# Performance work log

Hardware: AMD Instinct MI355X
Metric: run time of the kernel (lower is better)

The kernel has to match this reference:

```python
import jax, jax.numpy as jnp
import numpy as np
import math

N, S, T, E, H = 2, 2048, 2048, 1024, 16
HD = E // H  # head_dim = 64


def setup_inputs() -> dict:
    key = jax.random.key(0)
    ks = jax.random.split(key, 11)
    scale = 1.0 / math.sqrt(E)
    inp = {
        "query": jax.random.normal(ks[0], (N, S, E), jnp.float32),
        "key": jax.random.normal(ks[1], (N, T, E), jnp.float32),
        "value": jax.random.normal(ks[2], (N, T, E), jnp.float32),
        "Wq": jax.random.normal(ks[3], (E, E), jnp.float32) * scale,
        "bq": jnp.zeros((E,), jnp.float32),
        "Wk": jax.random.normal(ks[4], (E, E), jnp.float32) * scale,
        "bk": jnp.zeros((E,), jnp.float32),
        "Wv": jax.random.normal(ks[5], (E, E), jnp.float32) * scale,
        "bv": jnp.zeros((E,), jnp.float32),
        "Wo": jax.random.normal(ks[6], (E, E), jnp.float32) * scale,
        "bo": jnp.zeros((E,), jnp.float32),
    }
    return inp


def reference(query, key, value, Wq, bq, Wk, bk, Wv, bv, Wo, bo):
    # QKV projections, then split heads: [N, S, E] -> [N, H, S, HD]
    q = (query @ Wq + bq).reshape(N, S, H, HD).transpose(0, 2, 1, 3)
    k = (key @ Wk + bk).reshape(N, T, H, HD).transpose(0, 2, 1, 3)
    v = (value @ Wv + bv).reshape(N, T, H, HD).transpose(0, 2, 1, 3)
    # scaled dot-product attention scores [N, H, S, T]
    scores = jnp.einsum('nhse,nhte->nhst', q, k) / math.sqrt(HD)
    attn = jax.nn.softmax(scores, axis=-1)
    # dropout is identity in eval mode
    out = jnp.einsum('nhst,nhte->nhse', attn, v)  # [N, H, S, HD]
    out = out.transpose(0, 2, 1, 3).reshape(N, S, E)
    return out @ Wo + bo
```

## Files before the change

### kernel.cpp

```cpp
#include <hip/hip_runtime.h>
#include <hip/hip_bf16.h>

typedef __bf16 bf16x8 __attribute__((ext_vector_type(8)));
typedef __bf16 bf16x4 __attribute__((ext_vector_type(4)));
typedef float  f32x4  __attribute__((ext_vector_type(4)));
typedef float  f32x16 __attribute__((ext_vector_type(16)));

#define MFMA16(a, b, c) __builtin_amdgcn_mfma_f32_16x16x32_bf16((a), (b), (c), 0, 0, 0)
#define MFMA32(a, b, c) __builtin_amdgcn_mfma_f32_32x32x16_bf16((a), (b), (c), 0, 0, 0)

constexpr int SEQ = 2048, EMB = 1024, NHEAD = 16, HD = 64;
constexpr float SSCALE = 0.18033688f;

__device__ __forceinline__ void glds16(const void* g, void* l) {
    __builtin_amdgcn_global_load_lds(
        (const __attribute__((address_space(1))) void*)g,
        (__attribute__((address_space(3))) void*)l, 16, 0, 0);
}

__global__ __launch_bounds__(256)
void prep(const float* __restrict__ W0, const float* __restrict__ W1,
          const float* __restrict__ W2, const float* __restrict__ W3,
          __bf16* __restrict__ T0, __bf16* __restrict__ T1,
          __bf16* __restrict__ T2, __bf16* __restrict__ T3,
          const float* __restrict__ X0, const float* __restrict__ X1,
          const float* __restrict__ X2, __bf16* __restrict__ Y0,
          __bf16* __restrict__ Y1, __bf16* __restrict__ Y2)
{
    __shared__ float tile[32][33];
    const int z = blockIdx.z;
    if (z < 4) {
        const float* W = (z==0) ? W0 : (z==1) ? W1 : (z==2) ? W2 : W3;
        __bf16*      T = (z==0) ? T0 : (z==1) ? T1 : (z==2) ? T2 : T3;
        const float s = (z == 0) ? SSCALE : 1.0f;
        const int kb = blockIdx.x * 32, nb = blockIdx.y * 32;
        const int c = threadIdx.x & 31, r0 = threadIdx.x >> 5;
#pragma unroll
        for (int i = 0; i < 4; ++i)
            tile[r0 + 8*i][c] = W[(size_t)(kb + r0 + 8*i)*1024 + nb + c];
        __syncthreads();
#pragma unroll
        for (int i = 0; i < 4; ++i)
            T[(size_t)(nb + r0 + 8*i)*1024 + kb + c] = (__bf16)(tile[c][r0 + 8*i] * s);
    } else {
        const float* X = (z==4) ? X0 : (z==5) ? X1 : X2;
        __bf16*      Y = (z==4) ? Y0 : (z==5) ? Y1 : Y2;
        const size_t base =
            ((size_t)(blockIdx.y * 32 + blockIdx.x) * 256 + threadIdx.x) * 16;
#pragma unroll
        for (int j = 0; j < 2; ++j) {
            const float4* s4 = (const float4*)(X + base + j*8);
            float4 f0 = s4[0], f1 = s4[1];
            bf16x8 v;
            v[0]=(__bf16)f0.x; v[1]=(__bf16)f0.y; v[2]=(__bf16)f0.z; v[3]=(__bf16)f0.w;
            v[4]=(__bf16)f1.x; v[5]=(__bf16)f1.y; v[6]=(__bf16)f1.z; v[7]=(__bf16)f1.w;
            *(bf16x8*)(Y + base + j*8) = v;
        }
    }
}

struct GArg { const __bf16* A; const __bf16* Bt; const float* bias; void* C;
              int mode; int kbase; int kcount; float bscale; };
struct GArgs3 { GArg a[3]; };

__global__ __launch_bounds__(256)
void gemmk(GArgs3 args)
{
    const GArg g = args.a[blockIdx.z];
    __shared__ __attribute__((aligned(16))) __bf16 As[128*64];
    __shared__ __attribute__((aligned(16))) __bf16 Bs[128*64];
    const int tid = threadIdx.x, lane = tid & 63, wave = tid >> 6;
    const int wm = wave >> 1, wn = wave & 1;
    const int quad = lane >> 4, l16 = lane & 15;
    const int bm = blockIdx.x, bn = blockIdx.y;

    f32x4 acc[4][4] = {};

    for (int kt = 0; kt < g.kcount; ++kt) {
        const int k0 = g.kbase + kt*64;
        __syncthreads();
#pragma unroll
        for (int j = 0; j < 4; ++j) {
            const int ci = j*256 + tid;
            const int row = ci >> 3, cg = ((ci & 7) ^ (row & 7)) * 8;
            glds16(g.A + (size_t)(bm*128 + row)*1024 + k0 + cg,
                   &As[(j*256 + wave*64)*8]);
        }
#pragma unroll
        for (int j = 0; j < 4; ++j) {
            const int ci = j*256 + tid;
            const int row = ci >> 3, cg = ((ci & 7) ^ (row & 7)) * 8;
            glds16(g.Bt + (size_t)(bn*128 + row)*1024 + k0 + cg,
                   &Bs[(j*256 + wave*64)*8]);
        }
        __syncthreads();
#pragma unroll
        for (int ks = 0; ks < 2; ++ks) {
            const int kc = ks*4 + quad;
            bf16x8 af[4], bfr[4];
#pragma unroll
            for (int mt = 0; mt < 4; ++mt) {
                const int ar = wm*64 + mt*16 + l16;
                af[mt] = *(const bf16x8*)&As[ar*64 + (kc ^ (ar & 7))*8];
            }
#pragma unroll
            for (int nt = 0; nt < 4; ++nt) {
                const int br = wn*64 + nt*16 + l16;
                bfr[nt] = *(const bf16x8*)&Bs[br*64 + (kc ^ (br & 7))*8];
            }
#pragma unroll
            for (int mt = 0; mt < 4; ++mt)
#pragma unroll
                for (int nt = 0; nt < 4; ++nt)
                    acc[mt][nt] = MFMA16(af[mt], bfr[nt], acc[mt][nt]);
        }
    }

#pragma unroll
    for (int nt = 0; nt < 4; ++nt) {
        const int n = bn*128 + wn*64 + nt*16 + l16;
        const float bvs = (g.bias ? g.bias[n] : 0.f) * g.bscale;
#pragma unroll
        for (int mt = 0; mt < 4; ++mt) {
            const int mbase = bm*128 + wm*64 + mt*16 + quad*4;
            f32x4 v = acc[mt][nt];
            if (g.mode == 0) {
                __bf16* C = (__bf16*)g.C;
                const int h = n >> 6, d = n & 63;
#pragma unroll
                for (int r = 0; r < 4; ++r) {
                    const int m = mbase + r;
                    const int nb = m >> 11, s = m & 2047;
                    C[(size_t)(nb*NHEAD + h)*(SEQ*HD) + (size_t)s*HD + d] = (__bf16)(v[r] + bvs);
                }
            } else {
                __bf16* C = (__bf16*)g.C;
                const int h = n >> 6, d = n & 63;
                const int nb = mbase >> 11, s = mbase & 2047;
                const int tg = (s >> 2) & 7;
                const int pg = (tg & 4) | ((tg & 1) << 1) | ((tg & 2) >> 1);
                const int sp = (s & ~31) | (pg << 2);
                bf16x4 o;
#pragma unroll
                for (int r = 0; r < 4; ++r) o[r] = (__bf16)(v[r] + bvs);
                *(bf16x4*)&C[(size_t)(nb*NHEAD + h)*(SEQ*HD) + (size_t)d*SEQ + sp] = o;
            }
        }
    }
}

__global__ __launch_bounds__(256)
void gemmo(const __bf16* __restrict__ A, const __bf16* __restrict__ Bt,
           const float* __restrict__ bias, float* __restrict__ C)
{
    __shared__ __attribute__((aligned(16))) __bf16 As[64*64];
    __shared__ __attribute__((aligned(16))) __bf16 Bs[128*64];
    const int tid = threadIdx.x, lane = tid & 63, wave = tid >> 6;
    const int quad = lane >> 4, l16 = lane & 15;
    const int bm = blockIdx.x, bn = blockIdx.y;

    f32x4 acc[4][2] = {};

    for (int k0 = 0; k0 < 1024; k0 += 64) {
        __syncthreads();
#pragma unroll
        for (int j = 0; j < 2; ++j) {
            const int ci = j*256 + tid;
            const int row = ci >> 3, cg = ((ci & 7) ^ (row & 7)) * 8;
            glds16(A + (size_t)(bm*64 + row)*1024 + k0 + cg,
                   &As[(j*256 + wave*64)*8]);
        }
#pragma unroll
        for (int j = 0; j < 4; ++j) {
            const int ci = j*256 + tid;
            const int row = ci >> 3, cg = ((ci & 7) ^ (row & 7)) * 8;
            glds16(Bt + (size_t)(bn*128 + row)*1024 + k0 + cg,
                   &Bs[(j*256 + wave*64)*8]);
        }
        __syncthreads();
#pragma unroll
        for (int ks = 0; ks < 2; ++ks) {
            const int kc = ks*4 + quad;
            bf16x8 af[4], bfr[2];
#pragma unroll
            for (int mt = 0; mt < 4; ++mt) {
                const int ar = mt*16 + l16;
                af[mt] = *(const bf16x8*)&As[ar*64 + (kc ^ (ar & 7))*8];
            }
#pragma unroll
            for (int nt = 0; nt < 2; ++nt) {
                const int br = wave*32 + nt*16 + l16;
                bfr[nt] = *(const bf16x8*)&Bs[br*64 + (kc ^ (br & 7))*8];
            }
#pragma unroll
            for (int mt = 0; mt < 4; ++mt)
#pragma unroll
                for (int nt = 0; nt < 2; ++nt)
                    acc[mt][nt] = MFMA16(af[mt], bfr[nt], acc[mt][nt]);
        }
    }
#pragma unroll
    for (int nt = 0; nt < 2; ++nt) {
        const int n = bn*128 + wave*32 + nt*16 + l16;
        const float bv = bias[n];
#pragma unroll
        for (int mt = 0; mt < 4; ++mt) {
            const int mbase = bm*64 + mt*16 + quad*4;
            f32x4 v = acc[mt][nt];
#pragma unroll
            for (int r = 0; r < 4; ++r)
                C[(size_t)(mbase + r)*1024 + n] = v[r] + bv;
        }
    }
}

__global__ __launch_bounds__(512, 2)
void attn32(const __bf16* __restrict__ qg, const __bf16* __restrict__ kg,
            const __bf16* __restrict__ vg, __bf16* __restrict__ Og)
{
    __shared__ __attribute__((aligned(16))) char smem[64*1024];
    float* Xch = (float*)smem;

    const int tid = threadIdx.x, lane = tid & 63, wave = tid >> 6;
    const int w4 = wave & 3, grp = wave >> 2;
    const int l32 = lane & 31, half = lane >> 5;
    const int nh = blockIdx.y;
    const int q0 = blockIdx.x * 128;
    const __bf16* qb = qg + (size_t)nh * (SEQ*HD);
    const __bf16* kb = kg + (size_t)nh * (SEQ*HD);
    const __bf16* vb = vg + (size_t)nh * (SEQ*HD);

    bf16x8 qf[4];
#pragma unroll
    for (int ks = 0; ks < 4; ++ks)
        qf[ks] = *(const bf16x8*)(qb + (size_t)(q0 + w4*32 + l32)*HD + ks*16 + half*8);

    bf16x8 vone;
#pragma unroll
    for (int i = 0; i < 8; ++i) vone[i] = (__bf16)1.0f;

    f32x16 oacc[2] = {};
    f32x16 osum = {};

    auto stage = [&](int b, int t0) {
        __bf16* Kd = (__bf16*)(smem + b * 16384);
        __bf16* Vd = (__bf16*)(smem + 32768 + b * 16384);
#pragma unroll
        for (int j = 0; j < 2; ++j) {
            const int ci = j*512 + tid;
            const int row = ci >> 3, cg = ((ci & 7) ^ (row & 7)) * 8;
            glds16(kb + (size_t)(t0 + row)*HD + cg, &Kd[(j*512 + wave*64)*8]);
        }
#pragma unroll
        for (int j = 0; j < 2; ++j) {
            const int ci = j*512 + tid;
            const int row = ci >> 4, pos = ci & 15;
            const int cg = ((pos & ~7) | ((pos & 7) ^ (row & 7))) * 8;
            glds16(vb + (size_t)row*SEQ + t0 + cg, &Vd[(j*512 + wave*64)*8]);
        }
    };

    stage(0, 0);
    int cur = 0;
    for (int it = 0; it < 16; ++it) {
        __syncthreads();
        if (it < 15) stage(cur ^ 1, (it + 1) * 128);

        const __bf16* Ks = (const __bf16*)(smem + cur * 16384);
        const __bf16* Vs = (const __bf16*)(smem + 32768 + cur * 16384);

        f32x16 sc[2] = {};
        __builtin_amdgcn_s_setprio(1);
#pragma unroll
        for (int ks = 0; ks < 4; ++ks) {
            const int c = ks*2 + half;
#pragma unroll
            for (int nt = 0; nt < 2; ++nt) {
                const int kr = grp*64 + nt*32 + l32;
                bf16x8 kf = *(const bf16x8*)&Ks[kr*64 + ((c ^ (kr & 7))*8)];
                sc[nt] = MFMA32(kf, qf[ks], sc[nt]);
            }
        }
        __builtin_amdgcn_s_setprio(0);

#pragma unroll
        for (int nt = 0; nt < 2; ++nt)
#pragma unroll
            for (int sub = 0; sub < 2; ++sub) {
                bf16x8 pf;
#pragma unroll
                for (int j = 0; j < 8; ++j)
                    pf[j] = (__bf16)exp2f(sc[nt][sub*8 + j]);
                const int c2 = grp*8 + (nt*2 + sub)*2 + half;
                __builtin_amdgcn_s_setprio(1);
#pragma unroll
                for (int dt = 0; dt < 2; ++dt) {
                    const int vr = dt*32 + l32;
                    const int pos = (c2 & ~7) | ((c2 & 7) ^ (vr & 7));
                    bf16x8 vf = *(const bf16x8*)&Vs[vr*128 + pos*8];
                    oacc[dt] = MFMA32(pf, vf, oacc[dt]);
                }
                osum = MFMA32(pf, vone, osum);
                __builtin_amdgcn_s_setprio(0);
            }
        cur ^= 1;
    }

    __syncthreads();
    if (grp == 1) {
        float* dst = &Xch[((w4*64) + lane) * 48];
#pragma unroll
        for (int i = 0; i < 16; ++i) {
            dst[i]      = oacc[0][i];
            dst[16 + i] = oacc[1][i];
            dst[32 + i] = osum[i];
        }
    }
    __syncthreads();
    if (grp == 0) {
        const float* src = &Xch[((w4*64) + lane) * 48];
#pragma unroll
        for (int i = 0; i < 16; ++i) {
            oacc[0][i] += src[i];
            oacc[1][i] += src[16 + i];
            osum[i]    += src[32 + i];
        }
        const int nb = nh >> 4, h = nh & 15;
#pragma unroll
        for (int reg = 0; reg < 16; ++reg) {
            const int row = (reg & 3) + 8*(reg >> 2) + 4*half;
            const int srow = q0 + w4*32 + row;
            const float inv = 1.0f / osum[reg];
#pragma unroll
            for (int dt = 0; dt < 2; ++dt)
                Og[(size_t)(nb*SEQ + srow)*EMB + h*HD + dt*32 + l32] =
                    (__bf16)(oacc[dt][reg] * inv);
        }
    }
}

extern "C" void kernel_launch(void* const* d_in, const int* in_sizes, int n_in,
                              void* d_out, int out_size, void* d_ws, size_t ws_size,
                              hipStream_t stream)
{
    const float* query = (const float*)d_in[0];
    const float* key_  = (const float*)d_in[1];
    const float* value = (const float*)d_in[2];
    const float* Wq = (const float*)d_in[3];
    const float* bq = (const float*)d_in[4];
    const float* Wk = (const float*)d_in[5];
    const float* bk = (const float*)d_in[6];
    const float* Wv = (const float*)d_in[7];
    const float* bv = (const float*)d_in[8];
    const float* Wo = (const float*)d_in[9];
    const float* bo = (const float*)d_in[10];
    float* out = (float*)d_out;

    constexpr size_t SZW = 1024u*1024u;
    constexpr size_t SZX = 4096u*1024u;
    __bf16* ws  = (__bf16*)d_ws;
    __bf16* WqT = ws;
    __bf16* WkT = WqT + SZW;
    __bf16* WvT = WkT + SZW;
    __bf16* WoT = WvT + SZW;
    __bf16* xv  = WoT + SZW;
    __bf16* qh  = xv + SZX;
    __bf16* kh  = qh + SZX;
    __bf16* vTh = kh + SZX;
    __bf16* xq  = (__bf16*)d_out;
    __bf16* xk  = xq + SZX;
    __bf16* Oh  = xv;

    prep<<<dim3(32, 32, 7), 256, 0, stream>>>(Wq, Wk, Wv, Wo, WqT, WkT, WvT, WoT,
                                              query, key_, value, xq, xk, xv);
    GArgs3 a;
    a.a[0] = { xq, WqT, bq, qh,  0, 0, 16, SSCALE };
    a.a[1] = { xk, WkT, bk, kh,  0, 0, 16, 1.0f };
    a.a[2] = { xv, WvT, bv, vTh, 1, 0, 16, 1.0f };
    gemmk<<<dim3(32, 8, 3), 256, 0, stream>>>(a);
    attn32<<<dim3(16, 32), 512, 0, stream>>>(qh, kh, vTh, Oh);
    gemmo<<<dim3(64, 8), 256, 0, stream>>>(Oh, WoT, bo, out);
}
```

Before: 231.1 us.

## Swizzle GEMM block order, precompute attention load pointers, use raw exp2 and packed bf16 convert

Both projection GEMMs now remap the linear block index so that consecutive blocks are spread across B column tiles, aiming for better L2 or cache locality across XCDs. The attention kernel precomputes the per-thread K/V global pointers once and advances them each tile, removing the address arithmetic from every staging step. The softmax exponent calls the raw hardware exp2 builtin instead of exp2f, which drops range handling, and packs pairs of floats to bf16 with v_cvt_pk_bf16_f32 inline asm. Together these target index overhead, conversion instruction count and memory locality, at the cost of relying on fixed grid shapes.

After: 211.6 us. 1.09x faster.

```diff
diff --git a/kernel.cpp b/kernel.cpp
--- a/kernel.cpp
+++ b/kernel.cpp
@@ -5,6 +5,7 @@
 typedef __bf16 bf16x4 __attribute__((ext_vector_type(4)));
 typedef float  f32x4  __attribute__((ext_vector_type(4)));
 typedef float  f32x16 __attribute__((ext_vector_type(16)));
+typedef unsigned int u32x4 __attribute__((ext_vector_type(4)));
 
 #define MFMA16(a, b, c) __builtin_amdgcn_mfma_f32_16x16x32_bf16((a), (b), (c), 0, 0, 0)
 #define MFMA32(a, b, c) __builtin_amdgcn_mfma_f32_32x32x16_bf16((a), (b), (c), 0, 0, 0)
@@ -66,13 +67,16 @@
 __global__ __launch_bounds__(256)
 void gemmk(GArgs3 args)
 {
-    const GArg g = args.a[blockIdx.z];
+    const int lin = blockIdx.x + (blockIdx.y << 5) + (blockIdx.z << 8);
+    const int nid = (lin & 7) * 96 + (lin >> 3);
+    const int gz = nid >> 8, rem = nid & 255;
+    const int bm = rem >> 3, bn = rem & 7;
+    const GArg g = args.a[gz];
     __shared__ __attribute__((aligned(16))) __bf16 As[128*64];
     __shared__ __attribute__((aligned(16))) __bf16 Bs[128*64];
     const int tid = threadIdx.x, lane = tid & 63, wave = tid >> 6;
     const int wm = wave >> 1, wn = wave & 1;
     const int quad = lane >> 4, l16 = lane & 15;
-    const int bm = blockIdx.x, bn = blockIdx.y;
 
     f32x4 acc[4][4] = {};
 
@@ -153,11 +157,13 @@
 void gemmo(const __bf16* __restrict__ A, const __bf16* __restrict__ Bt,
            const float* __restrict__ bias, float* __restrict__ C)
 {
+    const int lin = blockIdx.x + (blockIdx.y << 6);
+    const int nid = (lin & 7) * 64 + (lin >> 3);
+    const int bm = nid >> 3, bn = nid & 7;
     __shared__ __attribute__((aligned(16))) __bf16 As[64*64];
     __shared__ __attribute__((aligned(16))) __bf16 Bs[128*64];
     const int tid = threadIdx.x, lane = tid & 63, wave = tid >> 6;
     const int quad = lane >> 4, l16 = lane & 15;
-    const int bm = blockIdx.x, bn = blockIdx.y;
 
     f32x4 acc[4][2] = {};
 
@@ -242,29 +248,31 @@
     f32x16 oacc[2] = {};
     f32x16 osum = {};
 
-    auto stage = [&](int b, int t0) {
-        __bf16* Kd = (__bf16*)(smem + b * 16384);
-        __bf16* Vd = (__bf16*)(smem + 32768 + b * 16384);
-#pragma unroll
-        for (int j = 0; j < 2; ++j) {
-            const int ci = j*512 + tid;
-            const int row = ci >> 3, cg = ((ci & 7) ^ (row & 7)) * 8;
-            glds16(kb + (size_t)(t0 + row)*HD + cg, &Kd[(j*512 + wave*64)*8]);
-        }
-#pragma unroll
-        for (int j = 0; j < 2; ++j) {
-            const int ci = j*512 + tid;
-            const int row = ci >> 4, pos = ci & 15;
-            const int cg = ((pos & ~7) | ((pos & 7) ^ (row & 7))) * 8;
-            glds16(vb + (size_t)row*SEQ + t0 + cg, &Vd[(j*512 + wave*64)*8]);
-        }
+    const int cK0 = tid, rK0 = cK0 >> 3;
+    const int cK1 = 512 + tid, rK1 = cK1 >> 3;
+    const __bf16* kp0 = kb + (size_t)rK0*HD + ((cK0 & 7) ^ (rK0 & 7)) * 8;
+    const __bf16* kp1 = kb + (size_t)rK1*HD + ((cK1 & 7) ^ (rK1 & 7)) * 8;
+    const int cV0 = tid, rV0 = cV0 >> 4, pV0 = cV0 & 15;
+    const int cV1 = 512 + tid, rV1 = cV1 >> 4, pV1 = cV1 & 15;
+    const __bf16* vp0 = vb + (size_t)rV0*SEQ + (((pV0 & ~7) | ((pV0 & 7) ^ (rV0 & 7))) * 8);
+    const __bf16* vp1 = vb + (size_t)rV1*SEQ + (((pV1 & ~7) | ((pV1 & 7) ^ (rV1 & 7))) * 8);
+
+    auto stage = [&](int b) {
+        char* Kd = smem + b * 16384;
+        char* Vd = smem + 32768 + b * 16384;
+        glds16(kp0, Kd + wave*1024);
+        glds16(kp1, Kd + 8192 + wave*1024);
+        glds16(vp0, Vd + wave*1024);
+        glds16(vp1, Vd + 8192 + wave*1024);
+        kp0 += 128*HD; kp1 += 128*HD;
+        vp0 += 128;    vp1 += 128;
     };
 
-    stage(0, 0);
+    stage(0);
     int cur = 0;
     for (int it = 0; it < 16; ++it) {
         __syncthreads();
-        if (it < 15) stage(cur ^ 1, (it + 1) * 128);
+        if (it < 15) stage(cur ^ 1);
 
         const __bf16* Ks = (const __bf16*)(smem + cur * 16384);
         const __bf16* Vs = (const __bf16*)(smem + 32768 + cur * 16384);
@@ -287,10 +295,20 @@
         for (int nt = 0; nt < 2; ++nt)
 #pragma unroll
             for (int sub = 0; sub < 2; ++sub) {
-                bf16x8 pf;
-#pragma unroll
-                for (int j = 0; j < 8; ++j)
-                    pf[j] = (__bf16)exp2f(sc[nt][sub*8 + j]);
+                const float e0 = __builtin_amdgcn_exp2f(sc[nt][sub*8 + 0]);
+                const float e1 = __builtin_amdgcn_exp2f(sc[nt][sub*8 + 1]);
+                const float e2 = __builtin_amdgcn_exp2f(sc[nt][sub*8 + 2]);
+                const float e3 = __builtin_amdgcn_exp2f(sc[nt][sub*8 + 3]);
+                const float e4 = __builtin_amdgcn_exp2f(sc[nt][sub*8 + 4]);
+                const float e5 = __builtin_amdgcn_exp2f(sc[nt][sub*8 + 5]);
+                const float e6 = __builtin_amdgcn_exp2f(sc[nt][sub*8 + 6]);
+                const float e7 = __builtin_amdgcn_exp2f(sc[nt][sub*8 + 7]);
+                u32x4 pk;
+                asm("v_cvt_pk_bf16_f32 %0, %1, %2" : "=v"(pk.x) : "v"(e0), "v"(e1));
+                asm("v_cvt_pk_bf16_f32 %0, %1, %2" : "=v"(pk.y) : "v"(e2), "v"(e3));
+                asm("v_cvt_pk_bf16_f32 %0, %1, %2" : "=v"(pk.z) : "v"(e4), "v"(e5));
+                asm("v_cvt_pk_bf16_f32 %0, %1, %2" : "=v"(pk.w) : "v"(e6), "v"(e7));
+                const bf16x8 pf = __builtin_bit_cast(bf16x8, pk);
                 const int c2 = grp*8 + (nt*2 + sub)*2 + half;
                 __builtin_amdgcn_s_setprio(1);
 #pragma unroll
```
